# Performance work log

Measured on AMD Instinct MI355X. Metric: run time of the kernel, lower is better.

Reference implementation:

```python
import jax, jax.numpy as jnp
import numpy as np

ALPHA = 0.2   # LeakyReLU negative slope
BN_EPS = 1e-5
NEG_INF = -9e15  # same masking constant as the torch source


def make_quaternion_mul(kernel):
    # kernel: [in_features//4, out_features]; returns hamilton [in_features, out_features]
    r, i, j, k = jnp.split(kernel, 4, axis=1)
    r2 = jnp.concatenate([r, -i, -j, -k], axis=1)
    i2 = jnp.concatenate([i,  r, -k,  j], axis=1)
    j2 = jnp.concatenate([j,  k,  r, -i], axis=1)
    k2 = jnp.concatenate([k, -j,  i,  r], axis=1)
    return jnp.concatenate([r2, i2, j2, k2], axis=0)


def setup_inputs() -> dict:
    key = jax.random.key(0)
    k1, k2, k3, k4 = jax.random.split(key, 4)
    N, IN_F, OUT_F = 8192, 1024, 256
    inp = jax.random.normal(k1, (N, IN_F), dtype=jnp.float32)
    adj = jax.random.randint(k2, (N, N), 0, 2, dtype=jnp.int32)
    # xavier-uniform-like init scales
    W = jax.random.uniform(k3, (IN_F // 4, OUT_F), dtype=jnp.float32,
                           minval=-1.0, maxval=1.0) * np.sqrt(6.0 / (IN_F // 4 + OUT_F))
    a = jax.random.uniform(k4, (2 * OUT_F, 1), dtype=jnp.float32,
                           minval=-1.0, maxval=1.0) * np.sqrt(6.0 / (2 * OUT_F + 1))
    gamma = jnp.ones((OUT_F,), dtype=jnp.float32)
    beta = jnp.zeros((OUT_F,), dtype=jnp.float32)
    return {"input": inp, "adj": adj, "W": W, "a": a, "gamma": gamma, "beta": beta}


def reference(input, adj, W, a, gamma, beta):
    hamilton = make_quaternion_mul(W)            # [IN_F, OUT_F]
    h = input @ hamilton                         # [N, OUT_F]
    F_out = h.shape[1]
    # e[i, j] = leakyrelu(concat(h_i, h_j) . a) = leakyrelu(h_i.a1 + h_j.a2)
    a1 = a[:F_out, 0]
    a2 = a[F_out:, 0]
    e = jax.nn.leaky_relu((h @ a1)[:, None] + (h @ a2)[None, :],
                          negative_slope=ALPHA)  # [N, N]
    e = jnp.where(adj > 0, e, NEG_INF)
    attention = jax.nn.softmax(e, axis=1)        # masked softmax over neighbors
    h_prime = attention @ h                      # [N, OUT_F]
    # BatchNorm1d (training mode: batch statistics, biased variance)
    mean = jnp.mean(h_prime, axis=0)
    var = jnp.var(h_prime, axis=0)
    h_norm = (h_prime - mean) * jax.lax.rsqrt(var + BN_EPS) * gamma + beta
    return jax.nn.elu(h_norm)                    # concat=True -> elu
```

## Files before the change

### kernel.cpp

```cpp
#include <hip/hip_runtime.h>
#include <stdint.h>

#define ALPHA 0.2f
#define LOG2E 1.4426950408889634f

typedef __attribute__((ext_vector_type(8))) short short8;
typedef __attribute__((ext_vector_type(4))) float f32x4;
typedef __attribute__((ext_vector_type(4))) int int4v;
typedef __attribute__((ext_vector_type(2))) unsigned int uint2v;

#if __has_builtin(__builtin_amdgcn_exp2f)
#define EXP2(x) __builtin_amdgcn_exp2f(x)
#else
#define EXP2(x) exp2f(x)
#endif

__device__ __forceinline__ unsigned short f2bf(float x){
  union { float f; uint32_t u; } v; v.f = x;
  uint32_t u = v.u;
  u += 0x7FFFu + ((u >> 16) & 1u);
  return (unsigned short)(u >> 16);
}
__device__ __forceinline__ float bf2f(unsigned short s){
  union { uint32_t u; float f; } v; v.u = ((uint32_t)s) << 16; return v.f;
}
__device__ __forceinline__ unsigned encf(float x){
  unsigned u = __float_as_uint(x);
  return (u & 0x80000000u) ? ~u : (u | 0x80000000u);
}
__device__ __forceinline__ float decf(unsigned u){
  return (u & 0x80000000u) ? __uint_as_float(u & 0x7FFFFFFFu) : __uint_as_float(~u);
}

__global__ void k_ham(const float* __restrict__ W, unsigned short* __restrict__ hi,
                      unsigned short* __restrict__ lo){
  int id = blockIdx.x * 256 + threadIdx.x;
  int c = id >> 10, k = id & 1023;
  int b = k >> 8, r = k & 255;
  int cb = c >> 6, col = c & 63;
  const int   comp[4][4] = {{0,1,2,3},{1,0,3,2},{2,3,0,1},{3,2,1,0}};
  const float sgn [4][4] = {{1.f,-1.f,-1.f,-1.f},{1.f,1.f,-1.f,1.f},
                            {1.f,1.f,1.f,-1.f},{1.f,-1.f,1.f,1.f}};
  float v = sgn[b][cb] * W[r * 256 + comp[b][cb] * 64 + col];
  unsigned short h = f2bf(v);
  hi[id] = h;
  lo[id] = f2bf(v - bf2f(h));
}

__global__ void k_pack(const int* __restrict__ adj, unsigned long long* __restrict__ bm,
                       unsigned* __restrict__ S2enc, float* __restrict__ gsum,
                       float* __restrict__ gsumsq){
  if (blockIdx.x == 0){
    if (threadIdx.x == 0) S2enc[0] = 0u;
    gsum[threadIdx.x] = 0.f; gsumsq[threadIdx.x] = 0.f;
  }
  const int lane = threadIdx.x & 63;
  const size_t wid = ((size_t)blockIdx.x * 256 + threadIdx.x) >> 6;
  const size_t W0 = wid * 1024;
  unsigned long long b[16];
#pragma unroll
  for (int q = 0; q < 4; ++q){
    int4v a = *(const int4v*)(adj + W0 + 256*q + 4*lane);
#pragma unroll
    for (int k = 0; k < 4; ++k) b[4*q + k] = __ballot(a[k] > 0);
  }
  if (lane < 16){
    unsigned long long v = b[0];
#pragma unroll
    for (int m = 1; m < 16; ++m) v = (lane == m) ? b[m] : v;
    bm[W0/64 + lane] = v;
  }
}

__global__ __launch_bounds__(256) void k_gemm1(
    const float* __restrict__ inp, const unsigned short* __restrict__ hamHi,
    const unsigned short* __restrict__ hamLo, const float* __restrict__ avec,
    unsigned short* __restrict__ hT, float* __restrict__ s1s, float* __restrict__ s2s,
    unsigned* __restrict__ S2enc){
  int i0 = blockIdx.x * 32;
  int w = threadIdx.x >> 6, lane = threadIdx.x & 63;
  int mi = lane & 15, g = lane >> 4;
  int cbase = w * 64;
  f32x4 acc[2][4];
#pragma unroll
  for (int mf=0; mf<2; ++mf)
#pragma unroll
    for (int nf=0; nf<4; ++nf) acc[mf][nf] = (f32x4){0.f,0.f,0.f,0.f};

  for (int k0 = 0; k0 < 1024; k0 += 32){
    short8 ah[2], al[2];
#pragma unroll
    for (int mf=0; mf<2; ++mf){
      const float* ap = inp + (size_t)(i0 + 16*mf + mi) * 1024 + k0 + 8*g;
      f32x4 x0 = *(const f32x4*)ap;
      f32x4 x1 = *(const f32x4*)(ap + 4);
#pragma unroll
      for (int e=0; e<8; ++e){
        float x = (e < 4) ? x0[e] : x1[e-4];
        unsigned short h = f2bf(x);
        ah[mf][e] = (short)h;
        al[mf][e] = (short)f2bf(x - bf2f(h));
      }
    }
    short8 bh[4], bl[4];
#pragma unroll
    for (int nf=0; nf<4; ++nf){
      size_t off = (size_t)(cbase + 16*nf + mi) * 1024 + k0 + 8*g;
      bh[nf] = *(const short8*)(hamHi + off);
      bl[nf] = *(const short8*)(hamLo + off);
    }
#pragma unroll
    for (int mf=0; mf<2; ++mf)
#pragma unroll
      for (int nf=0; nf<4; ++nf){
        acc[mf][nf] = __builtin_amdgcn_mfma_f32_16x16x32_bf16(ah[mf], bh[nf], acc[mf][nf], 0,0,0);
        acc[mf][nf] = __builtin_amdgcn_mfma_f32_16x16x32_bf16(ah[mf], bl[nf], acc[mf][nf], 0,0,0);
        acc[mf][nf] = __builtin_amdgcn_mfma_f32_16x16x32_bf16(al[mf], bh[nf], acc[mf][nf], 0,0,0);
      }
  }
  float p1[2][4] = {{0,0,0,0},{0,0,0,0}}, p2[2][4] = {{0,0,0,0},{0,0,0,0}};
#pragma unroll
  for (int nf=0; nf<4; ++nf){
    int c = cbase + 16*nf + mi;
    float a1c = avec[c], a2c = avec[256 + c];
    int Sc = (c & 7) << 3;
#pragma unroll
    for (int mf=0; mf<2; ++mf){
      int ibase = i0 + 16*mf + 4*g;
      uint2v u;
      u[0] = (uint32_t)f2bf(acc[mf][nf][0]) | ((uint32_t)f2bf(acc[mf][nf][1]) << 16);
      u[1] = (uint32_t)f2bf(acc[mf][nf][2]) | ((uint32_t)f2bf(acc[mf][nf][3]) << 16);
      *(uint2v*)(hT + (size_t)c * 8192 + (size_t)(ibase ^ Sc)) = u;
#pragma unroll
      for (int rg=0; rg<4; ++rg){
        p1[mf][rg] += acc[mf][nf][rg] * a1c;
        p2[mf][rg] += acc[mf][nf][rg] * a2c;
      }
    }
  }
#pragma unroll
  for (int off=1; off<16; off<<=1){
#pragma unroll
    for (int mf=0; mf<2; ++mf)
#pragma unroll
      for (int rg=0; rg<4; ++rg){
        p1[mf][rg] += __shfl_xor(p1[mf][rg], off);
        p2[mf][rg] += __shfl_xor(p2[mf][rg], off);
      }
  }
  __shared__ float red1[4][32], red2[4][32];
  if (mi == 0){
#pragma unroll
    for (int mf=0; mf<2; ++mf)
#pragma unroll
      for (int rg=0; rg<4; ++rg){
        red1[w][16*mf + 4*g + rg] = p1[mf][rg];
        red2[w][16*mf + 4*g + rg] = p2[mf][rg];
      }
  }
  __syncthreads();
  if (threadIdx.x < 32){
    int r = threadIdx.x;
    float v1 = red1[0][r] + red1[1][r] + red1[2][r] + red1[3][r];
    float v2 = red2[0][r] + red2[1][r] + red2[2][r] + red2[3][r];
    s1s[i0 + r] = v1 * LOG2E;
    float v2s = v2 * LOG2E;
    s2s[i0 + r] = v2s;
    float m = v2s;
#pragma unroll
    for (int off=1; off<32; off<<=1) m = fmaxf(m, __shfl_xor(m, off));
    if (r == 0) atomicMax(S2enc, encf(m));
  }
}

#define STAGE(t, b) do { \
    _Pragma("unroll") \
    for (int r_ = 0; r_ < 4; ++r_){ \
      int ch_ = tid + r_*512; \
      const unsigned short* gp_ = hT + (size_t)(ch_ >> 3)*8192 + jw0 + (t)*64 + (ch_&7)*8; \
      __builtin_amdgcn_global_load_lds((const __attribute__((address_space(1))) void*)(const void*)gp_, \
          (__attribute__((address_space(3))) void*)(void*)&hbuf[(b)][tid*8 + r_*4096], 16, 0, 0); \
    } } while(0)

__global__ __launch_bounds__(512,2) void k_attn(
    const unsigned long long* __restrict__ bm, const unsigned short* __restrict__ hT,
    const float* __restrict__ s1s, const float* __restrict__ s2s,
    const unsigned* __restrict__ S2enc, float* __restrict__ accp, float* __restrict__ Zp){
  __shared__ unsigned short hbuf[2][256*64];
  __shared__ float s2l[2048];
  const int tid = threadIdx.x;
  const int id = blockIdx.x;
  const int js = (id & 7) >> 1;
  const int rb = ((id >> 3) << 1) | (id & 1);
  const int w = tid >> 6, lane = tid & 63;
  const int mi = lane & 15, g = lane >> 4;
  const int i0w = rb * 128 + w * 16;
  const int jw0 = js * 2048;

  { f32x4 v = *(const f32x4*)(s2s + jw0 + tid*4); *(f32x4*)&s2l[tid*4] = v; }

  float S2MAX = decf(S2enc[0]);
  float s1v = s1s[i0w + mi];
  float xm = s1v + S2MAX;
  float m2 = fmaxf(xm, ALPHA * xm);

  const unsigned long long* brow = bm + (size_t)(i0w + mi) * 128 + (jw0 >> 8) * 4;

  f32x4 acc[16];
#pragma unroll
  for (int nf=0; nf<16; ++nf) acc[nf] = (f32x4){0.f,0.f,0.f,0.f};
  float zac = 0.f;

  unsigned long long Wc[4], Wn[4];
#pragma unroll
  for (int k=0;k<4;++k) Wc[k] = brow[k];
  STAGE(0, 0);
  __syncthreads();

  for (int tile = 0; tile < 32; ++tile){
    const int buf = tile & 1;
    if ((tile & 3) == 0){
      if (tile){
#pragma unroll
        for (int k=0;k<4;++k) Wc[k] = Wn[k];
      }
      if (tile + 4 < 32){
        const unsigned long long* p = brow + (tile >> 2)*4 + 4;
#pragma unroll
        for (int k=0;k<4;++k) Wn[k] = p[k];
      }
    }
    if (tile < 31) STAGE(tile + 1, buf ^ 1);
    const int base16 = (tile & 3) << 4;
#pragma unroll
    for (int ks=0; ks<2; ++ks){
      f32x4 sa = *(const f32x4*)&s2l[tile*64 + ks*32 + 8*g];
      f32x4 sb = *(const f32x4*)&s2l[tile*64 + ks*32 + 8*g + 4];
      const int sh0 = base16 + ks*8 + 2*g;
      unsigned tt[4];
#pragma unroll
      for (int k=0;k<4;++k) tt[k] = (unsigned)(Wc[k] >> sh0);
      short8 pa;
#pragma unroll
      for (int e=0; e<8; ++e){
        float s2e = (e < 4) ? sa[e] : sb[e-4];
        float x = s1v + s2e;
        float t = fmaxf(x, ALPHA * x);
        float pe = EXP2(t - m2);
        pe = ((tt[e & 3] >> (e >> 2)) & 1u) ? pe : 0.f;
        zac += pe;
        pa[e] = (short)f2bf(pe);
      }
      const int goff = ((4*ks + g) ^ (mi & 7)) << 3;
#pragma unroll
      for (int nf=0; nf<16; ++nf){
        short8 b = *(const short8*)&hbuf[buf][(16*nf + mi)*64 + goff];
        acc[nf] = __builtin_amdgcn_mfma_f32_16x16x32_bf16(pa, b, acc[nf], 0,0,0);
      }
    }
    __syncthreads();
  }
  {
    float z = zac;
    z += __shfl_xor(z, 16);
    z += __shfl_xor(z, 32);
    if (lane < 16) Zp[js*8192 + i0w + lane] = z;
  }
#pragma unroll
  for (int nf=0; nf<16; ++nf){
    int c = 16*nf + mi;
#pragma unroll
    for (int rg=0; rg<4; ++rg)
      accp[(size_t)(js*8192 + i0w + 4*g + rg)*256 + c] = acc[nf][rg];
  }
}

__global__ void k_stats(const float* __restrict__ accp, const float* __restrict__ Zp,
                        float* __restrict__ hp, float* __restrict__ gsum,
                        float* __restrict__ gsumsq){
  int c = threadIdx.x;
  int r0 = blockIdx.x * 32;
  float s = 0.f, sq = 0.f;
  for (int r=0; r<32; ++r){
    int i = r0 + r;
    float z = Zp[i] + Zp[8192 + i] + Zp[16384 + i] + Zp[24576 + i];
    float inv = (z > 0.f) ? 1.f / z : 0.f;
    size_t o = (size_t)i * 256 + c;
    float v = (accp[o] + accp[o + 8192*256] + accp[o + 2*8192*256] + accp[o + 3*8192*256]) * inv;
    hp[o] = v;
    s += v; sq += v*v;
  }
  atomicAdd(&gsum[c], s);
  atomicAdd(&gsumsq[c], sq);
}

__global__ void k_bnelu(float* __restrict__ out, const float* __restrict__ gsum,
                        const float* __restrict__ gsumsq, const float* __restrict__ gamma,
                        const float* __restrict__ beta){
  int id = blockIdx.x * 256 + threadIdx.x;
  int c = id & 255;
  float mean = gsum[c] * (1.f/8192.f);
  float var  = gsumsq[c] * (1.f/8192.f) - mean*mean;
  float x = (out[id] - mean) * rsqrtf(var + 1e-5f) * gamma[c] + beta[c];
  out[id] = x > 0.f ? x : (EXP2(x * LOG2E) - 1.f);
}

extern "C" void kernel_launch(void* const* d_in, const int* in_sizes, int n_in,
                              void* d_out, int out_size, void* d_ws, size_t ws_size,
                              hipStream_t stream){
  const float* inp   = (const float*)d_in[0];
  const int*   adj   = (const int*)d_in[1];
  const float* W     = (const float*)d_in[2];
  const float* avec  = (const float*)d_in[3];
  const float* gamma = (const float*)d_in[4];
  const float* beta  = (const float*)d_in[5];
  float* out = (float*)d_out;

  char* ws = (char*)d_ws;
  float* accp = (float*)ws;
  float* Zp   = accp + 4*8192*256;
  unsigned short* hamHi = (unsigned short*)(Zp + 32768);
  unsigned short* hamLo = hamHi + 262144;
  unsigned short* hT    = hamLo + 262144;
  float* s1s = (float*)(hT + 2097152);
  float* s2s = s1s + 8192;
  unsigned* S2enc = (unsigned*)(s2s + 8192);
  float* gsum   = (float*)(S2enc + 64);
  float* gsumsq = gsum + 256;
  unsigned long long* bm = (unsigned long long*)(gsumsq + 256);

  k_ham<<<1024, 256, 0, stream>>>(W, hamHi, hamLo);
  k_pack<<<16384, 256, 0, stream>>>(adj, bm, S2enc, gsum, gsumsq);
  k_gemm1<<<256, 256, 0, stream>>>(inp, hamHi, hamLo, avec, hT, s1s, s2s, S2enc);
  k_attn<<<256, 512, 0, stream>>>(bm, hT, s1s, s2s, S2enc, accp, Zp);
  k_stats<<<256, 256, 0, stream>>>(accp, Zp, out, gsum, gsumsq);
  k_bnelu<<<8192, 256, 0, stream>>>(out, gsum, gsumsq, gamma, beta);
}
```

Measured before the change: 183.0 us.

## Fuse adjacency mask read into attention kernel and switch to 32x32 MFMA

Drops the separate bitmask-packing kernel and has the attention kernel read the int32 adjacency rows directly, double-buffered in registers alongside the LDS staging of h. The attention tile moves to 256 threads with 32 rows per wave using 32x32x16 bf16 MFMA instead of 16x16x32. The LeakyReLU is refactored into a max of two affine terms with the subtraction folded in. The goal is to avoid one launch and an extra pass over the mask. The cost is that attention now streams the full 256MB int adjacency instead of a 8MB bitmask, and occupancy drops to 1 block of 256 threads.

Measured after the change: 192.9 us. 1.05x slower.

```diff
diff --git a/kernel.cpp b/kernel.cpp
--- a/kernel.cpp
+++ b/kernel.cpp
@@ -6,6 +6,7 @@
 
 typedef __attribute__((ext_vector_type(8))) short short8;
 typedef __attribute__((ext_vector_type(4))) float f32x4;
+typedef __attribute__((ext_vector_type(16))) float f32x16;
 typedef __attribute__((ext_vector_type(4))) int int4v;
 typedef __attribute__((ext_vector_type(2))) unsigned int uint2v;
 
@@ -33,7 +34,12 @@
 }
 
 __global__ void k_ham(const float* __restrict__ W, unsigned short* __restrict__ hi,
-                      unsigned short* __restrict__ lo){
+                      unsigned short* __restrict__ lo, unsigned* __restrict__ S2enc,
+                      float* __restrict__ gsum, float* __restrict__ gsumsq){
+  if (blockIdx.x == 0){
+    if (threadIdx.x == 0) S2enc[0] = 0u;
+    gsum[threadIdx.x] = 0.f; gsumsq[threadIdx.x] = 0.f;
+  }
   int id = blockIdx.x * 256 + threadIdx.x;
   int c = id >> 10, k = id & 1023;
   int b = k >> 8, r = k & 255;
@@ -47,31 +53,6 @@
   lo[id] = f2bf(v - bf2f(h));
 }
 
-__global__ void k_pack(const int* __restrict__ adj, unsigned long long* __restrict__ bm,
-                       unsigned* __restrict__ S2enc, float* __restrict__ gsum,
-                       float* __restrict__ gsumsq){
-  if (blockIdx.x == 0){
-    if (threadIdx.x == 0) S2enc[0] = 0u;
-    gsum[threadIdx.x] = 0.f; gsumsq[threadIdx.x] = 0.f;
-  }
-  const int lane = threadIdx.x & 63;
-  const size_t wid = ((size_t)blockIdx.x * 256 + threadIdx.x) >> 6;
-  const size_t W0 = wid * 1024;
-  unsigned long long b[16];
-#pragma unroll
-  for (int q = 0; q < 4; ++q){
-    int4v a = *(const int4v*)(adj + W0 + 256*q + 4*lane);
-#pragma unroll
-    for (int k = 0; k < 4; ++k) b[4*q + k] = __ballot(a[k] > 0);
-  }
-  if (lane < 16){
-    unsigned long long v = b[0];
-#pragma unroll
-    for (int m = 1; m < 16; ++m) v = (lane == m) ? b[m] : v;
-    bm[W0/64 + lane] = v;
-  }
-}
-
 __global__ __launch_bounds__(256) void k_gemm1(
     const float* __restrict__ inp, const unsigned short* __restrict__ hamHi,
     const unsigned short* __restrict__ hamLo, const float* __restrict__ avec,
@@ -175,15 +156,22 @@
 
 #define STAGE(t, b) do { \
     _Pragma("unroll") \
-    for (int r_ = 0; r_ < 4; ++r_){ \
-      int ch_ = tid + r_*512; \
+    for (int r_ = 0; r_ < 8; ++r_){ \
+      int ch_ = tid + r_*256; \
       const unsigned short* gp_ = hT + (size_t)(ch_ >> 3)*8192 + jw0 + (t)*64 + (ch_&7)*8; \
       __builtin_amdgcn_global_load_lds((const __attribute__((address_space(1))) void*)(const void*)gp_, \
-          (__attribute__((address_space(3))) void*)(void*)&hbuf[(b)][tid*8 + r_*4096], 16, 0, 0); \
+          (__attribute__((address_space(3))) void*)(void*)&hbuf[(b)][ch_*8], 16, 0, 0); \
     } } while(0)
 
-__global__ __launch_bounds__(512,2) void k_attn(
-    const unsigned long long* __restrict__ bm, const unsigned short* __restrict__ hT,
+#define ALOAD(dst, t) do { \
+    _Pragma("unroll") \
+    for (int ks_ = 0; ks_ < 4; ++ks_){ \
+      dst[2*ks_]   = *(const int4v*)(arow + (t)*64 + ks_*16); \
+      dst[2*ks_+1] = *(const int4v*)(arow + (t)*64 + ks_*16 + 4); \
+    } } while(0)
+
+__global__ __launch_bounds__(256,1) void k_attn(
+    const int* __restrict__ adj, const unsigned short* __restrict__ hT,
     const float* __restrict__ s1s, const float* __restrict__ s2s,
     const unsigned* __restrict__ S2enc, float* __restrict__ accp, float* __restrict__ Zp){
   __shared__ unsigned short hbuf[2][256*64];
@@ -193,85 +181,81 @@
   const int js = (id & 7) >> 1;
   const int rb = ((id >> 3) << 1) | (id & 1);
   const int w = tid >> 6, lane = tid & 63;
-  const int mi = lane & 15, g = lane >> 4;
-  const int i0w = rb * 128 + w * 16;
+  const int r31 = lane & 31, hi = lane >> 5;
+  const int i0w = rb * 128 + w * 32;
   const int jw0 = js * 2048;
 
-  { f32x4 v = *(const f32x4*)(s2s + jw0 + tid*4); *(f32x4*)&s2l[tid*4] = v; }
-
-  float S2MAX = decf(S2enc[0]);
-  float s1v = s1s[i0w + mi];
-  float xm = s1v + S2MAX;
-  float m2 = fmaxf(xm, ALPHA * xm);
-
-  const unsigned long long* brow = bm + (size_t)(i0w + mi) * 128 + (jw0 >> 8) * 4;
-
-  f32x4 acc[16];
-#pragma unroll
-  for (int nf=0; nf<16; ++nf) acc[nf] = (f32x4){0.f,0.f,0.f,0.f};
+  { f32x4 v0 = *(const f32x4*)(s2s + jw0 + tid*8);
+    f32x4 v1 = *(const f32x4*)(s2s + jw0 + tid*8 + 4);
+    *(f32x4*)&s2l[tid*8] = v0; *(f32x4*)&s2l[tid*8 + 4] = v1; }
+
+  const float S2MAX = decf(S2enc[0]);
+  const float s1v = s1s[i0w + r31];
+  const float xm = s1v + S2MAX;
+  const float m2 = fmaxf(xm, ALPHA * xm);
+  const float P1 = s1v - m2;
+  const float P2 = ALPHA * s1v - m2;
+
+  const int* arow = adj + (size_t)(i0w + r31) * 8192 + jw0 + hi*8;
+
+  f32x16 acc[8];
+#pragma unroll
+  for (int nf=0; nf<8; ++nf)
+#pragma unroll
+    for (int q=0; q<16; ++q) acc[nf][q] = 0.f;
   float zac = 0.f;
 
-  unsigned long long Wc[4], Wn[4];
-#pragma unroll
-  for (int k=0;k<4;++k) Wc[k] = brow[k];
+  int4v cur[8], nxt[8];
+  ALOAD(cur, 0);
   STAGE(0, 0);
   __syncthreads();
 
   for (int tile = 0; tile < 32; ++tile){
     const int buf = tile & 1;
-    if ((tile & 3) == 0){
-      if (tile){
-#pragma unroll
-        for (int k=0;k<4;++k) Wc[k] = Wn[k];
-      }
-      if (tile + 4 < 32){
-        const unsigned long long* p = brow + (tile >> 2)*4 + 4;
-#pragma unroll
-        for (int k=0;k<4;++k) Wn[k] = p[k];
-      }
-    }
-    if (tile < 31) STAGE(tile + 1, buf ^ 1);
-    const int base16 = (tile & 3) << 4;
-#pragma unroll
-    for (int ks=0; ks<2; ++ks){
-      f32x4 sa = *(const f32x4*)&s2l[tile*64 + ks*32 + 8*g];
-      f32x4 sb = *(const f32x4*)&s2l[tile*64 + ks*32 + 8*g + 4];
-      const int sh0 = base16 + ks*8 + 2*g;
-      unsigned tt[4];
-#pragma unroll
-      for (int k=0;k<4;++k) tt[k] = (unsigned)(Wc[k] >> sh0);
+    if (tile < 31){
+      STAGE(tile + 1, buf ^ 1);
+      ALOAD(nxt, tile + 1);
+    }
+#pragma unroll
+    for (int ks=0; ks<4; ++ks){
+      f32x4 sa = *(const f32x4*)&s2l[tile*64 + ks*16 + hi*8];
+      f32x4 sb = *(const f32x4*)&s2l[tile*64 + ks*16 + hi*8 + 4];
       short8 pa;
 #pragma unroll
       for (int e=0; e<8; ++e){
         float s2e = (e < 4) ? sa[e] : sb[e-4];
-        float x = s1v + s2e;
-        float t = fmaxf(x, ALPHA * x);
-        float pe = EXP2(t - m2);
-        pe = ((tt[e & 3] >> (e >> 2)) & 1u) ? pe : 0.f;
+        float t1 = P1 + s2e;
+        float t2 = fmaf(ALPHA, s2e, P2);
+        float pe = EXP2(fmaxf(t1, t2));
+        int ae = (e < 4) ? cur[2*ks][e] : cur[2*ks+1][e-4];
+        pe = (ae > 0) ? pe : 0.f;
         zac += pe;
         pa[e] = (short)f2bf(pe);
       }
-      const int goff = ((4*ks + g) ^ (mi & 7)) << 3;
-#pragma unroll
-      for (int nf=0; nf<16; ++nf){
-        short8 b = *(const short8*)&hbuf[buf][(16*nf + mi)*64 + goff];
-        acc[nf] = __builtin_amdgcn_mfma_f32_16x16x32_bf16(pa, b, acc[nf], 0,0,0);
-      }
+      const int xk = ks*16 + hi*8;
+#pragma unroll
+      for (int nf=0; nf<8; ++nf){
+        const int c = 32*nf + r31;
+        short8 b = *(const short8*)&hbuf[buf][c*64 + (xk ^ ((c&7)<<3))];
+        acc[nf] = __builtin_amdgcn_mfma_f32_32x32x16_bf16(pa, b, acc[nf], 0,0,0);
+      }
+    }
+    if (tile < 31){
+#pragma unroll
+      for (int q=0; q<8; ++q) cur[q] = nxt[q];
     }
     __syncthreads();
   }
-  {
-    float z = zac;
-    z += __shfl_xor(z, 16);
-    z += __shfl_xor(z, 32);
-    if (lane < 16) Zp[js*8192 + i0w + lane] = z;
-  }
-#pragma unroll
-  for (int nf=0; nf<16; ++nf){
-    int c = 16*nf + mi;
-#pragma unroll
-    for (int rg=0; rg<4; ++rg)
-      accp[(size_t)(js*8192 + i0w + 4*g + rg)*256 + c] = acc[nf][rg];
+  zac += __shfl_xor(zac, 32);
+  if (lane < 32) Zp[js*8192 + i0w + lane] = zac;
+#pragma unroll
+  for (int nf=0; nf<8; ++nf){
+    const int c = 32*nf + r31;
+#pragma unroll
+    for (int reg=0; reg<16; ++reg){
+      const int roff = (reg&3) + 8*(reg>>2) + 4*hi;
+      accp[(size_t)(js*8192 + i0w + roff)*256 + c] = acc[nf][reg];
+    }
   }
 }
 
@@ -327,12 +311,10 @@
   unsigned* S2enc = (unsigned*)(s2s + 8192);
   float* gsum   = (float*)(S2enc + 64);
   float* gsumsq = gsum + 256;
-  unsigned long long* bm = (unsigned long long*)(gsumsq + 256);
-
-  k_ham<<<1024, 256, 0, stream>>>(W, hamHi, hamLo);
-  k_pack<<<16384, 256, 0, stream>>>(adj, bm, S2enc, gsum, gsumsq);
+
+  k_ham<<<1024, 256, 0, stream>>>(W, hamHi, hamLo, S2enc, gsum, gsumsq);
   k_gemm1<<<256, 256, 0, stream>>>(inp, hamHi, hamLo, avec, hT, s1s, s2s, S2enc);
-  k_attn<<<256, 512, 0, stream>>>(bm, hT, s1s, s2s, S2enc, accp, Zp);
+  k_attn<<<256, 256, 0, stream>>>(adj, hT, s1s, s2s, S2enc, accp, Zp);
   k_stats<<<256, 256, 0, stream>>>(accp, Zp, out, gsum, gsumsq);
   k_bnelu<<<8192, 256, 0, stream>>>(out, gsum, gsumsq, gamma, beta);
 }
```
